# Kernel optimization log

Hardware: AMD Instinct MI355X
Metric: run time of the kernel (lower is better)

The kernel has to match this reference:

```python
import jax, jax.numpy as jnp
import numpy as np

EPS = 1e-08


def _center(K):
    # H K H with H = I - 11^T/n, expressed as O(n^2) double mean-subtraction
    rm = K.mean(axis=-1, keepdims=True)
    cm = K.mean(axis=-2, keepdims=True)
    tm = K.mean(axis=(-1, -2), keepdims=True)
    return K - rm - cm + tm


def setup_inputs() -> dict:
    key = jax.random.key(0)
    k1, k2 = jax.random.split(key)
    L, B, n, d = 5, 8, 1024, 64
    teacher = jax.random.normal(k1, (L, B, n, d), dtype=jnp.float32)
    student = jax.random.normal(k2, (L, B, n, d), dtype=jnp.float32)
    return {"teacher": teacher, "student": student}


def reference(teacher, student):
    # teacher, student: [L, B, n, d]  (internal=True, dim>=3 branch)
    cX = _center(jnp.einsum('lbnd,lbmd->lbnm', teacher, teacher))  # [L,B,n,n]
    cY = _center(jnp.einsum('lbnd,lbmd->lbnm', student, student))  # [L,B,n,n]
    hsic_xy = jnp.sum(cX * cY, axis=(-1, -2))  # [L,B]
    var_x = jnp.sqrt(jnp.sum(cX * cX, axis=(-1, -2)))  # [L,B]
    var_y = jnp.sqrt(jnp.sum(cY * cY, axis=(-1, -2)))  # [L,B]
    ratio = jnp.abs(hsic_xy / (var_x * var_y))  # [L,B]
    loss_per_layer = -jnp.log(ratio.mean(axis=-1) + EPS)  # [L]
    return loss_per_layer.mean()  # sum over layers / length
```

## Files before the change

kernel.cpp:

```cpp
#include <hip/hip_runtime.h>
#include <math.h>

#define LL 5
#define BB 8
#define NN 1024
#define DD 64
#define LB (LL * BB)
#define SPLIT 16
#define KC (NN / SPLIT)
#define ZC (2 * DD)
#define NQ 3

#define GP_SZ (LB * SPLIT * NQ * 4096)
#define SP_SZ (LB * SPLIT * ZC)
#define ACC_OFF (GP_SZ + SP_SZ)

typedef short short8 __attribute__((ext_vector_type(8)));
typedef float floatx4 __attribute__((ext_vector_type(4)));

__device__ __forceinline__ unsigned short f2bf(float f) {
    union { float f; unsigned u; } v; v.f = f;
    const unsigned u = v.u;
    return (unsigned short)((u + 0x7FFFu + ((u >> 16) & 1u)) >> 16);
}
__device__ __forceinline__ float bf2f(unsigned short h) {
    union { unsigned u; float f; } v; v.u = ((unsigned)h) << 16; return v.f;
}

__device__ __forceinline__ short8 read_frag(const short* Zt, int tbase, int lane, int k0) {
    const int c = tbase + (lane & 15);
    const int o = (k0 >> 3) + (lane >> 4);
    return *(const short8*)(Zt + c * 64 + ((o ^ (c & 7)) << 3));
}

__global__ __launch_bounds__(256) void gram_kernel(const float* __restrict__ X,
                                                   const float* __restrict__ Y,
                                                   float* __restrict__ Gp,
                                                   float* __restrict__ Sp) {
    __shared__ short Zt[ZC * KC];
    __shared__ float cscr[8][ZC];

    const int lb = blockIdx.y, nc = blockIdx.x, tid = threadIdx.x;
    const int r0 = nc * KC;
    const float4* X4 = (const float4*)(X + (size_t)lb * NN * DD);
    const float4* Y4 = (const float4*)(Y + (size_t)lb * NN * DD);

    const int col4 = tid & 31;
    float4 v[8];
#pragma unroll
    for (int m = 0; m < 8; ++m) {
        const int row = (tid >> 5) + 8 * m;
        v[m] = (col4 < 16) ? X4[(size_t)(r0 + row) * 16 + col4]
                           : Y4[(size_t)(r0 + row) * 16 + (col4 - 16)];
    }

    float cs[4] = {0.f, 0.f, 0.f, 0.f};
#pragma unroll
    for (int m = 0; m < 8; ++m) {
        const int k = (tid >> 5) + 8 * m;
        const float a[4] = {v[m].x, v[m].y, v[m].z, v[m].w};
#pragma unroll
        for (int e = 0; e < 4; ++e) {
            const int c = 4 * col4 + e;
            const unsigned short b = f2bf(a[e]);
            cs[e] += bf2f(b);
            Zt[c * 64 + (((k >> 3) ^ (c & 7)) << 3) + (k & 7)] = (short)b;
        }
    }
#pragma unroll
    for (int e = 0; e < 4; ++e) cscr[tid >> 5][4 * col4 + e] = cs[e];
    __syncthreads();
    if (tid < ZC) {
        float s = 0.f;
#pragma unroll
        for (int g = 0; g < 8; ++g) s += cscr[g][tid];
        Sp[(lb * SPLIT + nc) * ZC + tid] = s;
    }

    const int lane = tid & 63, w = tid >> 6;
    const int wr = (w >> 1) * 64, wc = (w & 1) * 64;

    floatx4 acc[4][4];
#pragma unroll
    for (int i = 0; i < 4; ++i)
#pragma unroll
        for (int j = 0; j < 4; ++j) acc[i][j] = (floatx4){0.f, 0.f, 0.f, 0.f};

#pragma unroll
    for (int k0 = 0; k0 < KC; k0 += 32) {
        short8 af[4], bfr[4];
#pragma unroll
        for (int i = 0; i < 4; ++i) af[i] = read_frag(Zt, wr + i * 16, lane, k0);
#pragma unroll
        for (int j = 0; j < 4; ++j) bfr[j] = read_frag(Zt, wc + j * 16, lane, k0);
#pragma unroll
        for (int i = 0; i < 4; ++i)
#pragma unroll
            for (int j = 0; j < 4; ++j)
                acc[i][j] = __builtin_amdgcn_mfma_f32_16x16x32_bf16(af[i], bfr[j], acc[i][j], 0, 0, 0);
    }

    if (w != 2) {
        const int slot = (w == 0) ? 0 : (w == 1) ? 1 : 2;
        float* Gb = Gp + ((size_t)(lb * SPLIT + nc) * NQ + slot) * 4096;
        const int g = lane >> 4, cl = lane & 15;
#pragma unroll
        for (int i = 0; i < 4; ++i)
#pragma unroll
            for (int j = 0; j < 4; ++j)
#pragma unroll
                for (int r = 0; r < 4; ++r)
                    Gb[(i * 16 + g * 4 + r) * 64 + (j * 16 + cl)] = acc[i][j][r];
    }
}

__global__ __launch_bounds__(256) void reduce_kernel(const float* __restrict__ Gp,
                                                     const float* __restrict__ Sp,
                                                     float* __restrict__ Acc) {
    const int b = blockIdx.x;
    const int lb = b / (NQ * 4);
    const int rem = b % (NQ * 4);
    const int q = rem >> 2, seg = rem & 3;
    const int tid = threadIdx.x;

    __shared__ float stot[ZC];
    __shared__ float red[4];

    if (tid < ZC) {
        float s = 0.f;
#pragma unroll
        for (int sp = 0; sp < SPLIT; ++sp) s += Sp[(lb * SPLIT + sp) * ZC + tid];
        stot[tid] = s;
    }
    __syncthreads();

    const int rowbase = (q == 2) ? 64 : 0;
    const int colbase = (q == 0) ? 0 : 64;
    const int idx0 = seg * 1024 + tid * 4;

    float4 g = make_float4(0.f, 0.f, 0.f, 0.f);
#pragma unroll
    for (int sp = 0; sp < SPLIT; ++sp) {
        const float4 p = *(const float4*)&Gp[((size_t)(lb * SPLIT + sp) * NQ + q) * 4096 + idx0];
        g.x += p.x; g.y += p.y; g.z += p.z; g.w += p.w;
    }
    const int row = idx0 >> 6, colb = idx0 & 63;
    const float inv_n = 1.0f / (float)NN;
    const float srow = stot[rowbase + row] * inv_n;
    const float ga[4] = {g.x, g.y, g.z, g.w};
    float sq = 0.f;
#pragma unroll
    for (int e = 0; e < 4; ++e) {
        const float cv = ga[e] - srow * stot[colbase + colb + e];
        sq += cv * cv;
    }
#pragma unroll
    for (int off = 32; off; off >>= 1) sq += __shfl_down(sq, off);
    const int wave = tid >> 6;
    if ((tid & 63) == 0) red[wave] = sq;
    __syncthreads();
    if (tid == 0)
        atomicAdd(&Acc[lb * 4 + q], red[0] + red[1] + red[2] + red[3]);
}

__global__ void final_kernel(const float* __restrict__ Acc, float* __restrict__ out) {
    const int tid = threadIdx.x;
    float v = 0.0f;
    if (tid < LB) {
        const float a = Acc[tid * 4 + 0];
        const float h = Acc[tid * 4 + 1];
        const float bb = Acc[tid * 4 + 2];
        v = fabsf(h / (sqrtf(a) * sqrtf(bb)));
    }
    v += __shfl_xor(v, 1);
    v += __shfl_xor(v, 2);
    v += __shfl_xor(v, 4);
    float loss = 0.0f;
#pragma unroll
    for (int l = 0; l < LL; ++l) {
        const float sl = __shfl(v, l * BB);
        loss += -logf(sl * (1.0f / (float)BB) + 1e-8f);
    }
    if (tid == 0) out[0] = loss * (1.0f / (float)LL);
}

extern "C" void kernel_launch(void* const* d_in, const int* in_sizes, int n_in,
                              void* d_out, int out_size, void* d_ws, size_t ws_size,
                              hipStream_t stream) {
    const float* teacher = (const float*)d_in[0];
    const float* student = (const float*)d_in[1];
    float* ws = (float*)d_ws;
    float* Gp = ws;
    float* Sp = ws + GP_SZ;
    float* Acc = ws + ACC_OFF;

    hipMemsetAsync(Acc, 0, LB * 4 * sizeof(float), stream);

    dim3 grid1(SPLIT, LB);
    gram_kernel<<<grid1, 256, 0, stream>>>(teacher, student, Gp, Sp);
    reduce_kernel<<<LB * NQ * 4, 256, 0, stream>>>(Gp, Sp, Acc);
    final_kernel<<<1, 64, 0, stream>>>(Acc, (float*)d_out);
}
```

Measured before the change: 82.62 us.

## Rework gram tile split, vectorize LDS staging, drop memset and atomics

```diff
diff --git a/kernel.cpp b/kernel.cpp
--- a/kernel.cpp
+++ b/kernel.cpp
@@ -5,7 +5,7 @@
 #define BB 8
 #define NN 1024
 #define DD 64
-#define LB (LL * BB)
+#define LB 40
 #define SPLIT 16
 #define KC (NN / SPLIT)
 #define ZC (2 * DD)
@@ -30,7 +30,8 @@
 __device__ __forceinline__ short8 read_frag(const short* Zt, int tbase, int lane, int k0) {
     const int c = tbase + (lane & 15);
     const int o = (k0 >> 3) + (lane >> 4);
-    return *(const short8*)(Zt + c * 64 + ((o ^ (c & 7)) << 3));
+    const int oct = (o ^ ((c + (c >> 4)) & 15)) & 7;
+    return *(const short8*)(Zt + c * 64 + (oct << 3));
 }
 
 __global__ __launch_bounds__(256) void gram_kernel(const float* __restrict__ X,
@@ -46,29 +47,31 @@
     const float4* Y4 = (const float4*)(Y + (size_t)lb * NN * DD);
 
     const int col4 = tid & 31;
+    const int rb = tid >> 5;
     float4 v[8];
 #pragma unroll
     for (int m = 0; m < 8; ++m) {
-        const int row = (tid >> 5) + 8 * m;
+        const int row = 8 * rb + m;
         v[m] = (col4 < 16) ? X4[(size_t)(r0 + row) * 16 + col4]
                            : Y4[(size_t)(r0 + row) * 16 + (col4 - 16)];
     }
 
-    float cs[4] = {0.f, 0.f, 0.f, 0.f};
-#pragma unroll
-    for (int m = 0; m < 8; ++m) {
-        const int k = (tid >> 5) + 8 * m;
-        const float a[4] = {v[m].x, v[m].y, v[m].z, v[m].w};
-#pragma unroll
-        for (int e = 0; e < 4; ++e) {
-            const int c = 4 * col4 + e;
-            const unsigned short b = f2bf(a[e]);
-            cs[e] += bf2f(b);
-            Zt[c * 64 + (((k >> 3) ^ (c & 7)) << 3) + (k & 7)] = (short)b;
+#pragma unroll
+    for (int e = 0; e < 4; ++e) {
+        const int c = 4 * col4 + e;
+        short8 w8;
+        float cs = 0.f;
+#pragma unroll
+        for (int m = 0; m < 8; ++m) {
+            const float fv = (e == 0) ? v[m].x : (e == 1) ? v[m].y : (e == 2) ? v[m].z : v[m].w;
+            const unsigned short b = f2bf(fv);
+            cs += bf2f(b);
+            w8[m] = (short)b;
         }
-    }
-#pragma unroll
-    for (int e = 0; e < 4; ++e) cscr[tid >> 5][4 * col4 + e] = cs[e];
+        const int oct = (rb ^ ((c + (c >> 4)) & 15)) & 7;
+        *(short8*)(Zt + c * 64 + (oct << 3)) = w8;
+        cscr[rb][c] = cs;
+    }
     __syncthreads();
     if (tid < ZC) {
         float s = 0.f;
@@ -78,45 +81,60 @@
     }
 
     const int lane = tid & 63, w = tid >> 6;
-    const int wr = (w >> 1) * 64, wc = (w & 1) * 64;
-
-    floatx4 acc[4][4];
-#pragma unroll
-    for (int i = 0; i < 4; ++i)
-#pragma unroll
-        for (int j = 0; j < 4; ++j) acc[i][j] = (floatx4){0.f, 0.f, 0.f, 0.f};
+
+    floatx4 acc[2][8];
+#pragma unroll
+    for (int i = 0; i < 2; ++i)
+#pragma unroll
+        for (int j = 0; j < 8; ++j) acc[i][j] = (floatx4){0.f, 0.f, 0.f, 0.f};
 
 #pragma unroll
     for (int k0 = 0; k0 < KC; k0 += 32) {
-        short8 af[4], bfr[4];
-#pragma unroll
-        for (int i = 0; i < 4; ++i) af[i] = read_frag(Zt, wr + i * 16, lane, k0);
-#pragma unroll
-        for (int j = 0; j < 4; ++j) bfr[j] = read_frag(Zt, wc + j * 16, lane, k0);
-#pragma unroll
-        for (int i = 0; i < 4; ++i)
-#pragma unroll
-            for (int j = 0; j < 4; ++j)
+        short8 af[2], bfr[8];
+#pragma unroll
+        for (int i = 0; i < 2; ++i) af[i] = read_frag(Zt, (2 * w + i) * 16, lane, k0);
+#pragma unroll
+        for (int j = 0; j < 8; ++j) bfr[j] = read_frag(Zt, j * 16, lane, k0);
+#pragma unroll
+        for (int i = 0; i < 2; ++i)
+#pragma unroll
+            for (int j = 0; j < 8; ++j)
                 acc[i][j] = __builtin_amdgcn_mfma_f32_16x16x32_bf16(af[i], bfr[j], acc[i][j], 0, 0, 0);
     }
 
-    if (w != 2) {
-        const int slot = (w == 0) ? 0 : (w == 1) ? 1 : 2;
-        float* Gb = Gp + ((size_t)(lb * SPLIT + nc) * NQ + slot) * 4096;
-        const int g = lane >> 4, cl = lane & 15;
-#pragma unroll
-        for (int i = 0; i < 4; ++i)
-#pragma unroll
-            for (int j = 0; j < 4; ++j)
-#pragma unroll
-                for (int r = 0; r < 4; ++r)
-                    Gb[(i * 16 + g * 4 + r) * 64 + (j * 16 + cl)] = acc[i][j][r];
+    float* Gb = Gp + (size_t)(lb * SPLIT + nc) * (NQ * 4096);
+    const int g = lane >> 4, cl = lane & 15;
+    if (w < 2) {
+#pragma unroll
+        for (int i = 0; i < 2; ++i)
+#pragma unroll
+            for (int j = 0; j < 8; ++j) {
+                const int slab = (j < 4) ? 0 : 1;
+                const int qcol = (j & 3) * 16 + cl;
+#pragma unroll
+                for (int r = 0; r < 4; ++r) {
+                    const int qrow = (2 * w + i) * 16 + g * 4 + r;
+                    Gb[slab * 4096 + qrow * 64 + qcol] = acc[i][j][r];
+                }
+            }
+    } else {
+#pragma unroll
+        for (int i = 0; i < 2; ++i)
+#pragma unroll
+            for (int j = 4; j < 8; ++j) {
+                const int qcol = (j - 4) * 16 + cl;
+#pragma unroll
+                for (int r = 0; r < 4; ++r) {
+                    const int qrow = (2 * (w - 2) + i) * 16 + g * 4 + r;
+                    Gb[2 * 4096 + qrow * 64 + qcol] = acc[i][j][r];
+                }
+            }
     }
 }
 
 __global__ __launch_bounds__(256) void reduce_kernel(const float* __restrict__ Gp,
                                                      const float* __restrict__ Sp,
-                                                     float* __restrict__ Acc) {
+                                                     float* __restrict__ Acc2) {
     const int b = blockIdx.x;
     const int lb = b / (NQ * 4);
     const int rem = b % (NQ * 4);
@@ -134,24 +152,23 @@
     }
     __syncthreads();
 
+    const int idx0 = seg * 256 + tid;
+    float4 g = make_float4(0.f, 0.f, 0.f, 0.f);
+#pragma unroll
+    for (int sp = 0; sp < SPLIT; ++sp) {
+        const float4 p = *(const float4*)&Gp[((size_t)(lb * SPLIT + sp) * NQ + q) * 4096 + idx0 * 4];
+        g.x += p.x; g.y += p.y; g.z += p.z; g.w += p.w;
+    }
+    const int row = idx0 >> 4, col0 = (idx0 & 15) * 4;
     const int rowbase = (q == 2) ? 64 : 0;
     const int colbase = (q == 0) ? 0 : 64;
-    const int idx0 = seg * 1024 + tid * 4;
-
-    float4 g = make_float4(0.f, 0.f, 0.f, 0.f);
-#pragma unroll
-    for (int sp = 0; sp < SPLIT; ++sp) {
-        const float4 p = *(const float4*)&Gp[((size_t)(lb * SPLIT + sp) * NQ + q) * 4096 + idx0];
-        g.x += p.x; g.y += p.y; g.z += p.z; g.w += p.w;
-    }
-    const int row = idx0 >> 6, colb = idx0 & 63;
     const float inv_n = 1.0f / (float)NN;
     const float srow = stot[rowbase + row] * inv_n;
     const float ga[4] = {g.x, g.y, g.z, g.w};
     float sq = 0.f;
 #pragma unroll
     for (int e = 0; e < 4; ++e) {
-        const float cv = ga[e] - srow * stot[colbase + colb + e];
+        const float cv = ga[e] - srow * stot[colbase + col0 + e];
         sq += cv * cv;
     }
 #pragma unroll
@@ -160,17 +177,21 @@
     if ((tid & 63) == 0) red[wave] = sq;
     __syncthreads();
     if (tid == 0)
-        atomicAdd(&Acc[lb * 4 + q], red[0] + red[1] + red[2] + red[3]);
-}
-
-__global__ void final_kernel(const float* __restrict__ Acc, float* __restrict__ out) {
+        Acc2[lb * 12 + q * 4 + seg] = red[0] + red[1] + red[2] + red[3];
+}
+
+__global__ void final_kernel(const float* __restrict__ Acc2, float* __restrict__ out) {
     const int tid = threadIdx.x;
     float v = 0.0f;
     if (tid < LB) {
-        const float a = Acc[tid * 4 + 0];
-        const float h = Acc[tid * 4 + 1];
-        const float bb = Acc[tid * 4 + 2];
-        v = fabsf(h / (sqrtf(a) * sqrtf(bb)));
+        float vxx = 0.f, hxy = 0.f, vyy = 0.f;
+#pragma unroll
+        for (int s = 0; s < 4; ++s) {
+            vxx += Acc2[tid * 12 + s];
+            hxy += Acc2[tid * 12 + 4 + s];
+            vyy += Acc2[tid * 12 + 8 + s];
+        }
+        v = fabsf(hxy / (sqrtf(vxx) * sqrtf(vyy)));
     }
     v += __shfl_xor(v, 1);
     v += __shfl_xor(v, 2);
@@ -192,12 +213,10 @@
     float* ws = (float*)d_ws;
     float* Gp = ws;
     float* Sp = ws + GP_SZ;
-    float* Acc = ws + ACC_OFF;
-
-    hipMemsetAsync(Acc, 0, LB * 4 * sizeof(float), stream);
+    float* Acc2 = ws + ACC_OFF;
 
     dim3 grid1(SPLIT, LB);
     gram_kernel<<<grid1, 256, 0, stream>>>(teacher, student, Gp, Sp);
-    reduce_kernel<<<LB * NQ * 4, 256, 0, stream>>>(Gp, Sp, Acc);
-    final_kernel<<<1, 64, 0, stream>>>(Acc, (float*)d_out);
-}
+    reduce_kernel<<<LB * NQ * 4, 256, 0, stream>>>(Gp, Sp, Acc2);
+    final_kernel<<<1, 64, 0, stream>>>(Acc2, (float*)d_out);
+}
```

Measured after the change: 78.08 us. 1.06x faster.
